# Performance work log

Measured on AMD Instinct MI355X. Metric: run time of the kernel, lower is better.

## Reference

```python
import jax, jax.numpy as jnp
import numpy as np

TEMPERATURE = 0.1

def setup_inputs() -> dict:
    key = jax.random.key(0)
    ks = jax.random.split(key, 6)
    B, K, D, H, N = 256, 32, 128, 256, 16
    z = jax.random.normal(ks[0], (B, K, D), dtype=jnp.float32)
    # edge MLP params: Linear(2D->H), GELU, Linear(H->D)
    W1 = jax.random.normal(ks[1], (2 * D, H), dtype=jnp.float32) * (1.0 / np.sqrt(2 * D))
    b1 = jnp.zeros((H,), dtype=jnp.float32)
    W2 = jax.random.normal(ks[2], (H, D), dtype=jnp.float32) * (1.0 / np.sqrt(H))
    b2 = jnp.zeros((D,), dtype=jnp.float32)
    codebook = jax.random.normal(ks[3], (N, D), dtype=jnp.float32) * 0.02
    return {"z": z, "W1": W1, "b1": b1, "W2": W2, "b2": b2, "codebook": codebook}

def reference(z, W1, b1, W2, b2, codebook):
    # z: (B,K,D). Edge MLP on concat([z_i, z_j]) == split-weight GEMMs,
    # avoiding materializing the (B,K,K,2D) concat tensor.
    D = z.shape[-1]
    h_i = jnp.einsum('bkd,dh->bkh', z, W1[:D])   # contribution of z_i
    h_j = jnp.einsum('bkd,dh->bkh', z, W1[D:])   # contribution of z_j
    h = h_i[:, :, None, :] + h_j[:, None, :, :] + b1       # (B,K,K,H)
    h = jax.nn.gelu(h, approximate=False)                    # torch nn.GELU default = exact erf
    e_ij = jnp.einsum('bijh,hd->bijd', h, W2) + b2           # (B,K,K,D)
    logits = jnp.einsum('bijd,nd->bijn', e_ij, codebook) / TEMPERATURE  # (B,K,K,N)
    alpha_ij = jax.nn.softmax(logits, axis=-1)
    m_ij = jnp.einsum('bijn,nd->bijd', alpha_ij, codebook)   # (B,K,K,D)
    return (m_ij, alpha_ij, e_ij, logits)
```

## Files before the change

### kernel.cpp

```cpp
#include <hip/hip_runtime.h>
#include <hip/hip_bf16.h>
#include <math.h>

#define BB 256
#define KK 32
#define DD 128
#define HH 256
#define NN 16
#define O0 ((size_t)0)
#define O1 ((size_t)33554432)
#define O2 ((size_t)37748736)
#define O3 ((size_t)71303168)

typedef float f32x4 __attribute__((ext_vector_type(4)));
typedef short s16x8 __attribute__((ext_vector_type(8)));

static __device__ __forceinline__ short f2bf(float x) {
  __hip_bfloat16 h = __float2bfloat16(x);
  return *reinterpret_cast<short*>(&h);
}
static __device__ __forceinline__ float bf2f(short s) {
  __hip_bfloat16 h;
  *reinterpret_cast<short*>(&h) = s;
  return __bfloat162float(h);
}
static __device__ __forceinline__ unsigned cvt_pk_bf16(float a, float b) {
  unsigned r;
  asm volatile("v_cvt_pk_bf16_f32 %0, %1, %2" : "=v"(r) : "v"(a), "v"(b));
  return r;
}

static __device__ __forceinline__ float gelu_exact(float x) {
  float ax = fabsf(x) * 0.70710678118654752f;
  float t = __builtin_amdgcn_rcpf(fmaf(0.3275911f, ax, 1.0f));
  float p = fmaf(1.061405429f, t, -1.453152027f);
  p = fmaf(p, t, 1.421413741f);
  p = fmaf(p, t, -0.284496736f);
  p = fmaf(p, t, 0.254829592f);
  p *= t;
  float e = __expf(-ax * ax);
  float er = fmaf(-p, e, 1.0f);
  er = copysignf(er, x);
  return 0.5f * x * (1.0f + er);
}

__global__ __launch_bounds__(256) void prep_kernel(
    const float* __restrict__ z, const float* __restrict__ W1,
    const float* __restrict__ W2, const float* __restrict__ cb,
    short* __restrict__ zb, short* __restrict__ W1th, short* __restrict__ W1tl,
    short* __restrict__ Wh, short* __restrict__ Wl,
    short* __restrict__ cbh, short* __restrict__ cbl, short* __restrict__ cbT) {
  const int idx = blockIdx.x * 256 + threadIdx.x;
  zb[idx] = f2bf(z[idx]);
  if (idx < 512 * 128) {
    int c = idx >> 7, k = idx & 127;
    float w = (c < 256) ? W1[(size_t)k * 256 + c]
                        : W1[(size_t)(128 + k) * 256 + (c - 256)];
    short h = f2bf(w);
    W1th[idx] = h;
    W1tl[idx] = f2bf(w - bf2f(h));
  }
  if (idx < 128 * 256) {
    int c = idx >> 8, k = idx & 255;
    float w = W2[(size_t)k * 128 + c];
    short h = f2bf(w);
    Wh[idx] = h;
    Wl[idx] = f2bf(w - bf2f(h));
  }
  if (idx < 2048) {
    float v = cb[idx];
    short h = f2bf(v);
    cbh[idx] = h;
    cbl[idx] = f2bf(v - bf2f(h));
  }
  if (idx < 128 * 32) {
    int c = idx >> 5, n = idx & 31;
    cbT[idx] = (n < 16) ? f2bf(cb[(size_t)n * 128 + c]) : (short)0;
  }
}

__global__ __launch_bounds__(256) void hproj_mfma(
    const short* __restrict__ zb, const short* __restrict__ W1th,
    const short* __restrict__ W1tl, const float* __restrict__ b1,
    float* __restrict__ H) {
  const int tid = threadIdx.x;
  const int lane = tid & 63;
  const int wv = tid >> 6;
  const int l4 = lane >> 4, l15 = lane & 15;
  const int row0 = blockIdx.x * 32;
  const int col0 = blockIdx.y * 128 + wv * 32;

  f32x4 acc[2][2];
#pragma unroll
  for (int mt = 0; mt < 2; ++mt)
#pragma unroll
    for (int nt = 0; nt < 2; ++nt)
      acc[mt][nt] = (f32x4){0.f, 0.f, 0.f, 0.f};

#pragma unroll
  for (int ks = 0; ks < 4; ++ks) {
    const int kof = ks * 32 + l4 * 8;
    s16x8 a0 = *(const s16x8*)(zb + (size_t)(row0 + l15) * 128 + kof);
    s16x8 a1 = *(const s16x8*)(zb + (size_t)(row0 + 16 + l15) * 128 + kof);
    s16x8 bh0 = *(const s16x8*)(W1th + (size_t)(col0 + l15) * 128 + kof);
    s16x8 bh1 = *(const s16x8*)(W1th + (size_t)(col0 + 16 + l15) * 128 + kof);
    s16x8 bl0 = *(const s16x8*)(W1tl + (size_t)(col0 + l15) * 128 + kof);
    s16x8 bl1 = *(const s16x8*)(W1tl + (size_t)(col0 + 16 + l15) * 128 + kof);
    acc[0][0] = __builtin_amdgcn_mfma_f32_16x16x32_bf16(a0, bh0, acc[0][0], 0, 0, 0);
    acc[0][0] = __builtin_amdgcn_mfma_f32_16x16x32_bf16(a0, bl0, acc[0][0], 0, 0, 0);
    acc[0][1] = __builtin_amdgcn_mfma_f32_16x16x32_bf16(a0, bh1, acc[0][1], 0, 0, 0);
    acc[0][1] = __builtin_amdgcn_mfma_f32_16x16x32_bf16(a0, bl1, acc[0][1], 0, 0, 0);
    acc[1][0] = __builtin_amdgcn_mfma_f32_16x16x32_bf16(a1, bh0, acc[1][0], 0, 0, 0);
    acc[1][0] = __builtin_amdgcn_mfma_f32_16x16x32_bf16(a1, bl0, acc[1][0], 0, 0, 0);
    acc[1][1] = __builtin_amdgcn_mfma_f32_16x16x32_bf16(a1, bh1, acc[1][1], 0, 0, 0);
    acc[1][1] = __builtin_amdgcn_mfma_f32_16x16x32_bf16(a1, bl1, acc[1][1], 0, 0, 0);
  }

#pragma unroll
  for (int nt = 0; nt < 2; ++nt) {
    const int col = col0 + nt * 16 + l15;
    const float bias = (col0 < 256) ? b1[col] : 0.f;
#pragma unroll
    for (int mt = 0; mt < 2; ++mt)
#pragma unroll
      for (int r = 0; r < 4; ++r)
        H[(size_t)(row0 + mt * 16 + l4 * 4 + r) * 512 + col] =
            acc[mt][nt][r] + bias;
  }
}

__global__ __launch_bounds__(256, 4) void pair_kernel(
    const float* __restrict__ Hcat, const short* __restrict__ Wh,
    const short* __restrict__ Wl, const float* __restrict__ b2,
    const short* __restrict__ cbh, const short* __restrict__ cbl,
    const short* __restrict__ cbT, float* __restrict__ out) {
  __shared__ short sAh[32 * 256];
  __shared__ union {
    short Al[32 * 256];
    struct { short Eh[32 * 128]; short El[32 * 128]; } e;
  } u;
  __shared__ short sAlp[32 * 32];

  const int tid = threadIdx.x;
  const int blk = blockIdx.x;
  const int b = blk >> 5;

  ((unsigned*)sAlp)[tid] = 0u;
  ((unsigned*)sAlp)[tid + 256] = 0u;

  {
    const int k0 = (tid & 127) * 2;
    const int pb = (tid >> 7) * 16;
    const float2 hiv = *(const float2*)(Hcat + (size_t)blk * 512 + k0);
    const float hx = hiv.x;
    const float hy = hiv.y;
    const float* hjp = Hcat + ((size_t)b * KK + pb) * 512 + 256 + k0;
    unsigned* aH = (unsigned*)sAh;
    unsigned* aL = (unsigned*)u.Al;
    const int cw = tid & 127;
#pragma unroll 4
    for (int p = 0; p < 16; ++p) {
      const int row = pb + p;
      float2 hj = *(const float2*)(hjp + (size_t)p * 512);
      float g0 = gelu_exact(hx + hj.x);
      float g1 = gelu_exact(hy + hj.y);
      unsigned h01 = cvt_pk_bf16(g0, g1);
      float h0f = __uint_as_float(h01 << 16);
      float h1f = __uint_as_float(h01 & 0xFFFF0000u);
      unsigned l01 = cvt_pk_bf16(g0 - h0f, g1 - h1f);
      const int wi = row * 128 + ((cw ^ ((row & 7) << 2)));
      aH[wi] = h01;
      aL[wi] = l01;
    }
  }
  __syncthreads();

  const int lane = tid & 63;
  const int wv = tid >> 6;
  const int nb = wv * 32;
  const int l4 = lane >> 4;
  const int l15 = lane & 15;

  f32x4 acc[2][2];
#pragma unroll
  for (int mt = 0; mt < 2; ++mt)
#pragma unroll
    for (int nt = 0; nt < 2; ++nt)
      acc[mt][nt] = (f32x4){0.f, 0.f, 0.f, 0.f};

  const int sw = (l15 & 7) << 4;
  const char* pAh = (const char*)sAh;
  const char* pAl = (const char*)u.Al;
  const size_t gB0 = (size_t)(nb + l15) * 256 + l4 * 8;

#pragma unroll
  for (int ks = 0; ks < 8; ++ks) {
    const int cbyte = ks * 64 + l4 * 16;
    const int o0 = l15 * 512 + (cbyte ^ sw);
    const int o1 = (16 + l15) * 512 + (cbyte ^ sw);
    s16x8 ah0 = *(const s16x8*)(pAh + o0);
    s16x8 ah1 = *(const s16x8*)(pAh + o1);
    s16x8 al0 = *(const s16x8*)(pAl + o0);
    s16x8 al1 = *(const s16x8*)(pAl + o1);
    const size_t g0 = gB0 + ks * 32;
    const size_t g1 = g0 + 16 * 256;
    s16x8 bh0 = *(const s16x8*)(Wh + g0);
    s16x8 bh1 = *(const s16x8*)(Wh + g1);
    s16x8 bl0 = *(const s16x8*)(Wl + g0);
    s16x8 bl1 = *(const s16x8*)(Wl + g1);

    acc[0][0] = __builtin_amdgcn_mfma_f32_16x16x32_bf16(ah0, bh0, acc[0][0], 0, 0, 0);
    acc[0][0] = __builtin_amdgcn_mfma_f32_16x16x32_bf16(al0, bh0, acc[0][0], 0, 0, 0);
    acc[0][0] = __builtin_amdgcn_mfma_f32_16x16x32_bf16(ah0, bl0, acc[0][0], 0, 0, 0);
    acc[0][1] = __builtin_amdgcn_mfma_f32_16x16x32_bf16(ah0, bh1, acc[0][1], 0, 0, 0);
    acc[0][1] = __builtin_amdgcn_mfma_f32_16x16x32_bf16(al0, bh1, acc[0][1], 0, 0, 0);
    acc[0][1] = __builtin_amdgcn_mfma_f32_16x16x32_bf16(ah0, bl1, acc[0][1], 0, 0, 0);
    acc[1][0] = __builtin_amdgcn_mfma_f32_16x16x32_bf16(ah1, bh0, acc[1][0], 0, 0, 0);
    acc[1][0] = __builtin_amdgcn_mfma_f32_16x16x32_bf16(al1, bh0, acc[1][0], 0, 0, 0);
    acc[1][0] = __builtin_amdgcn_mfma_f32_16x16x32_bf16(ah1, bl0, acc[1][0], 0, 0, 0);
    acc[1][1] = __builtin_amdgcn_mfma_f32_16x16x32_bf16(ah1, bh1, acc[1][1], 0, 0, 0);
    acc[1][1] = __builtin_amdgcn_mfma_f32_16x16x32_bf16(al1, bh1, acc[1][1], 0, 0, 0);
    acc[1][1] = __builtin_amdgcn_mfma_f32_16x16x32_bf16(ah1, bl1, acc[1][1], 0, 0, 0);
  }

  __syncthreads();

  {
    const float b2v0 = b2[nb + l15];
    const float b2v1 = b2[nb + 16 + l15];
    float* eg = out + O2 + (size_t)blk * (KK * DD);
    char* pEh = (char*)u.e.Eh;
    char* pEl = (char*)u.e.El;
#pragma unroll
    for (int mt = 0; mt < 2; ++mt) {
#pragma unroll
      for (int r = 0; r < 4; ++r) {
        const int row = mt * 16 + l4 * 4 + r;
        const int rsw = (row & 7) << 4;
        const float e0 = acc[mt][0][r] + b2v0;
        const float e1 = acc[mt][1][r] + b2v1;
        eg[row * 128 + nb + l15] = e0;
        eg[row * 128 + nb + 16 + l15] = e1;
        unsigned hp = cvt_pk_bf16(e0, e1);
        float h0f = __uint_as_float(hp << 16);
        float h1f = __uint_as_float(hp & 0xFFFF0000u);
        unsigned lp = cvt_pk_bf16(e0 - h0f, e1 - h1f);
        const int i0 = row * 256 + (((nb + l15) * 2) ^ rsw);
        const int i1 = row * 256 + (((nb + 16 + l15) * 2) ^ rsw);
        *(short*)(pEh + i0) = (short)(hp & 0xFFFFu);
        *(short*)(pEh + i1) = (short)(hp >> 16);
        *(short*)(pEl + i0) = (short)(lp & 0xFFFFu);
        *(short*)(pEl + i1) = (short)(lp >> 16);
      }
    }
  }
  __syncthreads();

  if (wv < 2) {
    const int mrow = wv * 16;
    f32x4 lacc = (f32x4){0.f, 0.f, 0.f, 0.f};
    const char* pEh = (const char*)u.e.Eh;
    const char* pEl = (const char*)u.e.El;
    const int rowa = mrow + l15;
    const int rsw = (rowa & 7) << 4;
#pragma unroll
    for (int ks = 0; ks < 4; ++ks) {
      const int cbyte = ks * 64 + l4 * 16;
      const int o = rowa * 256 + (cbyte ^ rsw);
      s16x8 eh = *(const s16x8*)(pEh + o);
      s16x8 el = *(const s16x8*)(pEl + o);
      const size_t g = (size_t)l15 * 128 + ks * 32 + l4 * 8;
      s16x8 ch = *(const s16x8*)(cbh + g);
      s16x8 cl = *(const s16x8*)(cbl + g);
      lacc = __builtin_amdgcn_mfma_f32_16x16x32_bf16(eh, ch, lacc, 0, 0, 0);
      lacc = __builtin_amdgcn_mfma_f32_16x16x32_bf16(el, ch, lacc, 0, 0, 0);
      lacc = __builtin_amdgcn_mfma_f32_16x16x32_bf16(eh, cl, lacc, 0, 0, 0);
    }
    float* lg_out = out + O3 + (size_t)blk * (KK * NN);
    float* ag_out = out + O1 + (size_t)blk * (KK * NN);
#pragma unroll
    for (int r = 0; r < 4; ++r) {
      const int row = mrow + l4 * 4 + r;
      float lg = lacc[r] * 10.0f;
      float mx = lg;
#pragma unroll
      for (int m = 1; m < 16; m <<= 1) mx = fmaxf(mx, __shfl_xor(mx, m));
      float p = __expf(lg - mx);
      float s = p;
#pragma unroll
      for (int m = 1; m < 16; m <<= 1) s += __shfl_xor(s, m);
      float a = p / s;
      lg_out[row * 16 + l15] = lg;
      ag_out[row * 16 + l15] = a;
      sAlp[row * 32 + l15] = f2bf(a);
    }
  }
  __syncthreads();

  {
    float* mg = out + O0 + (size_t)blk * (KK * DD);
#pragma unroll
    for (int rg = 0; rg < 2; ++rg) {
      s16x8 af = *(const s16x8*)(sAlp + (rg * 16 + l15) * 32 + l4 * 8);
#pragma unroll
      for (int nt = 0; nt < 2; ++nt) {
        const int c = nb + nt * 16 + l15;
        s16x8 bf = *(const s16x8*)(cbT + (size_t)c * 32 + l4 * 8);
        f32x4 mac = (f32x4){0.f, 0.f, 0.f, 0.f};
        mac = __builtin_amdgcn_mfma_f32_16x16x32_bf16(af, bf, mac, 0, 0, 0);
#pragma unroll
        for (int r = 0; r < 4; ++r)
          mg[(rg * 16 + l4 * 4 + r) * 128 + c] = mac[r];
      }
    }
  }
}

extern "C" void kernel_launch(void* const* d_in, const int* in_sizes, int n_in,
                              void* d_out, int out_size, void* d_ws, size_t ws_size,
                              hipStream_t stream) {
  const float* z  = (const float*)d_in[0];
  const float* W1 = (const float*)d_in[1];
  const float* b1 = (const float*)d_in[2];
  const float* W2 = (const float*)d_in[3];
  const float* b2 = (const float*)d_in[4];
  const float* cb = (const float*)d_in[5];
  float* out = (float*)d_out;

  float* Hcat = (float*)d_ws;
  short* zb   = (short*)(Hcat + (size_t)8192 * 512);
  short* W1th = zb + (size_t)1048576;
  short* W1tl = W1th + (size_t)65536;
  short* Wh   = W1tl + (size_t)65536;
  short* Wl   = Wh + (size_t)32768;
  short* cbh  = Wl + (size_t)32768;
  short* cbl  = cbh + (size_t)2048;
  short* cbT  = cbl + (size_t)2048;

  prep_kernel<<<4096, 256, 0, stream>>>(z, W1, W2, cb, zb, W1th, W1tl, Wh, Wl,
                                        cbh, cbl, cbT);
  hproj_mfma<<<dim3(256, 4), 256, 0, stream>>>(zb, W1th, W1tl, b1, Hcat);
  pair_kernel<<<BB * KK, 256, 0, stream>>>(Hcat, Wh, Wl, b2, cbh, cbl, cbT, out);
}
```

Baseline: 201.1 us.

## Fold W2·codebookᵀ into a precomputed matrix to compute logits directly from GELU activations

Precomputes V = W2·codebookᵀ (256x16) and b2·codebookᵀ in the prep kernel, so the pair kernel computes logits straight from the GELU tile inside the main MFMA loop. This removes the bf16 hi/lo staging of e_ij in shared memory, the second GEMM phase and two block barriers. The cost is extra MFMAs per k-step in every wave (each wave computes a redundant logit tile that only half the lanes store), larger LDS use since the union is gone, and lower occupancy from launch bounds changing 4 to 3. The per-thread serial 128-length dot products in the prep kernel add a small amount of work there.

```diff
diff --git a/kernel.cpp b/kernel.cpp
--- a/kernel.cpp
+++ b/kernel.cpp
@@ -47,9 +47,10 @@
 __global__ __launch_bounds__(256) void prep_kernel(
     const float* __restrict__ z, const float* __restrict__ W1,
     const float* __restrict__ W2, const float* __restrict__ cb,
+    const float* __restrict__ b2,
     short* __restrict__ zb, short* __restrict__ W1th, short* __restrict__ W1tl,
-    short* __restrict__ Wh, short* __restrict__ Wl,
-    short* __restrict__ cbh, short* __restrict__ cbl, short* __restrict__ cbT) {
+    short* __restrict__ Wh, short* __restrict__ Wl, short* __restrict__ cbT,
+    short* __restrict__ Vh, short* __restrict__ Vl, float* __restrict__ b2cb) {
   const int idx = blockIdx.x * 256 + threadIdx.x;
   zb[idx] = f2bf(z[idx]);
   if (idx < 512 * 128) {
@@ -67,15 +68,24 @@
     Wh[idx] = h;
     Wl[idx] = f2bf(w - bf2f(h));
   }
-  if (idx < 2048) {
-    float v = cb[idx];
-    short h = f2bf(v);
-    cbh[idx] = h;
-    cbl[idx] = f2bf(v - bf2f(h));
-  }
   if (idx < 128 * 32) {
     int c = idx >> 5, n = idx & 31;
     cbT[idx] = (n < 16) ? f2bf(cb[(size_t)n * 128 + c]) : (short)0;
+  }
+  if (idx < 16 * 256) {
+    int n = idx >> 8, k = idx & 255;
+    float s = 0.f;
+#pragma unroll 4
+    for (int c = 0; c < 128; ++c)
+      s += W2[(size_t)k * 128 + c] * cb[(size_t)n * 128 + c];
+    short h = f2bf(s);
+    Vh[idx] = h;
+    Vl[idx] = f2bf(s - bf2f(h));
+  }
+  if (idx < 16) {
+    float s = 0.f;
+    for (int c = 0; c < 128; ++c) s += b2[c] * cb[(size_t)idx * 128 + c];
+    b2cb[idx] = s;
   }
 }
 
@@ -129,16 +139,14 @@
   }
 }
 
-__global__ __launch_bounds__(256, 4) void pair_kernel(
+__global__ __launch_bounds__(256, 3) void pair_kernel(
     const float* __restrict__ Hcat, const short* __restrict__ Wh,
     const short* __restrict__ Wl, const float* __restrict__ b2,
-    const short* __restrict__ cbh, const short* __restrict__ cbl,
-    const short* __restrict__ cbT, float* __restrict__ out) {
+    const short* __restrict__ Vh, const short* __restrict__ Vl,
+    const float* __restrict__ b2cb, const short* __restrict__ cbT,
+    float* __restrict__ out) {
   __shared__ short sAh[32 * 256];
-  __shared__ union {
-    short Al[32 * 256];
-    struct { short Eh[32 * 128]; short El[32 * 128]; } e;
-  } u;
+  __shared__ short sAl[32 * 256];
   __shared__ short sAlp[32 * 32];
 
   const int tid = threadIdx.x;
@@ -156,7 +164,7 @@
     const float hy = hiv.y;
     const float* hjp = Hcat + ((size_t)b * KK + pb) * 512 + 256 + k0;
     unsigned* aH = (unsigned*)sAh;
-    unsigned* aL = (unsigned*)u.Al;
+    unsigned* aL = (unsigned*)sAl;
     const int cw = tid & 127;
 #pragma unroll 4
     for (int p = 0; p < 16; ++p) {
@@ -180,6 +188,7 @@
   const int nb = wv * 32;
   const int l4 = lane >> 4;
   const int l15 = lane & 15;
+  const int mtL = wv >> 1;
 
   f32x4 acc[2][2];
 #pragma unroll
@@ -187,11 +196,13 @@
 #pragma unroll
     for (int nt = 0; nt < 2; ++nt)
       acc[mt][nt] = (f32x4){0.f, 0.f, 0.f, 0.f};
+  f32x4 lacc = (f32x4){0.f, 0.f, 0.f, 0.f};
 
   const int sw = (l15 & 7) << 4;
   const char* pAh = (const char*)sAh;
-  const char* pAl = (const char*)u.Al;
+  const char* pAl = (const char*)sAl;
   const size_t gB0 = (size_t)(nb + l15) * 256 + l4 * 8;
+  const size_t gV0 = (size_t)l15 * 256 + l4 * 8;
 
 #pragma unroll
   for (int ks = 0; ks < 8; ++ks) {
@@ -221,67 +232,40 @@
     acc[1][1] = __builtin_amdgcn_mfma_f32_16x16x32_bf16(ah1, bh1, acc[1][1], 0, 0, 0);
     acc[1][1] = __builtin_amdgcn_mfma_f32_16x16x32_bf16(al1, bh1, acc[1][1], 0, 0, 0);
     acc[1][1] = __builtin_amdgcn_mfma_f32_16x16x32_bf16(ah1, bl1, acc[1][1], 0, 0, 0);
-  }
-
-  __syncthreads();
+
+    s16x8 vh = *(const s16x8*)(Vh + gV0 + ks * 32);
+    s16x8 vl = *(const s16x8*)(Vl + gV0 + ks * 32);
+    s16x8 aHm = mtL ? ah1 : ah0;
+    s16x8 aLm = mtL ? al1 : al0;
+    lacc = __builtin_amdgcn_mfma_f32_16x16x32_bf16(aHm, vh, lacc, 0, 0, 0);
+    lacc = __builtin_amdgcn_mfma_f32_16x16x32_bf16(aLm, vh, lacc, 0, 0, 0);
+    lacc = __builtin_amdgcn_mfma_f32_16x16x32_bf16(aHm, vl, lacc, 0, 0, 0);
+  }
 
   {
     const float b2v0 = b2[nb + l15];
     const float b2v1 = b2[nb + 16 + l15];
     float* eg = out + O2 + (size_t)blk * (KK * DD);
-    char* pEh = (char*)u.e.Eh;
-    char* pEl = (char*)u.e.El;
 #pragma unroll
     for (int mt = 0; mt < 2; ++mt) {
 #pragma unroll
       for (int r = 0; r < 4; ++r) {
         const int row = mt * 16 + l4 * 4 + r;
-        const int rsw = (row & 7) << 4;
-        const float e0 = acc[mt][0][r] + b2v0;
-        const float e1 = acc[mt][1][r] + b2v1;
-        eg[row * 128 + nb + l15] = e0;
-        eg[row * 128 + nb + 16 + l15] = e1;
-        unsigned hp = cvt_pk_bf16(e0, e1);
-        float h0f = __uint_as_float(hp << 16);
-        float h1f = __uint_as_float(hp & 0xFFFF0000u);
-        unsigned lp = cvt_pk_bf16(e0 - h0f, e1 - h1f);
-        const int i0 = row * 256 + (((nb + l15) * 2) ^ rsw);
-        const int i1 = row * 256 + (((nb + 16 + l15) * 2) ^ rsw);
-        *(short*)(pEh + i0) = (short)(hp & 0xFFFFu);
-        *(short*)(pEh + i1) = (short)(hp >> 16);
-        *(short*)(pEl + i0) = (short)(lp & 0xFFFFu);
-        *(short*)(pEl + i1) = (short)(lp >> 16);
+        eg[row * 128 + nb + l15] = acc[mt][0][r] + b2v0;
+        eg[row * 128 + nb + 16 + l15] = acc[mt][1][r] + b2v1;
       }
     }
   }
-  __syncthreads();
-
-  if (wv < 2) {
-    const int mrow = wv * 16;
-    f32x4 lacc = (f32x4){0.f, 0.f, 0.f, 0.f};
-    const char* pEh = (const char*)u.e.Eh;
-    const char* pEl = (const char*)u.e.El;
-    const int rowa = mrow + l15;
-    const int rsw = (rowa & 7) << 4;
-#pragma unroll
-    for (int ks = 0; ks < 4; ++ks) {
-      const int cbyte = ks * 64 + l4 * 16;
-      const int o = rowa * 256 + (cbyte ^ rsw);
-      s16x8 eh = *(const s16x8*)(pEh + o);
-      s16x8 el = *(const s16x8*)(pEl + o);
-      const size_t g = (size_t)l15 * 128 + ks * 32 + l4 * 8;
-      s16x8 ch = *(const s16x8*)(cbh + g);
-      s16x8 cl = *(const s16x8*)(cbl + g);
-      lacc = __builtin_amdgcn_mfma_f32_16x16x32_bf16(eh, ch, lacc, 0, 0, 0);
-      lacc = __builtin_amdgcn_mfma_f32_16x16x32_bf16(el, ch, lacc, 0, 0, 0);
-      lacc = __builtin_amdgcn_mfma_f32_16x16x32_bf16(eh, cl, lacc, 0, 0, 0);
-    }
+
+  {
+    const float b2cbv = b2cb[l15];
+    const bool own = ((l4 >> 1) == (wv & 1));
     float* lg_out = out + O3 + (size_t)blk * (KK * NN);
     float* ag_out = out + O1 + (size_t)blk * (KK * NN);
 #pragma unroll
     for (int r = 0; r < 4; ++r) {
-      const int row = mrow + l4 * 4 + r;
-      float lg = lacc[r] * 10.0f;
+      const int row = mtL * 16 + l4 * 4 + r;
+      float lg = (lacc[r] + b2cbv) * 10.0f;
       float mx = lg;
 #pragma unroll
       for (int m = 1; m < 16; m <<= 1) mx = fmaxf(mx, __shfl_xor(mx, m));
@@ -290,9 +274,11 @@
 #pragma unroll
       for (int m = 1; m < 16; m <<= 1) s += __shfl_xor(s, m);
       float a = p / s;
-      lg_out[row * 16 + l15] = lg;
-      ag_out[row * 16 + l15] = a;
-      sAlp[row * 32 + l15] = f2bf(a);
+      if (own) {
+        lg_out[row * 16 + l15] = lg;
+        ag_out[row * 16 + l15] = a;
+        sAlp[row * 32 + l15] = f2bf(a);
+      }
     }
   }
   __syncthreads();
@@ -333,12 +319,13 @@
   short* W1tl = W1th + (size_t)65536;
   short* Wh   = W1tl + (size_t)65536;
   short* Wl   = Wh + (size_t)32768;
-  short* cbh  = Wl + (size_t)32768;
-  short* cbl  = cbh + (size_t)2048;
-  short* cbT  = cbl + (size_t)2048;
-
-  prep_kernel<<<4096, 256, 0, stream>>>(z, W1, W2, cb, zb, W1th, W1tl, Wh, Wl,
-                                        cbh, cbl, cbT);
+  short* cbT  = Wl + (size_t)32768;
+  short* Vh   = cbT + (size_t)4096;
+  short* Vl   = Vh + (size_t)4096;
+  float* b2cb = (float*)(Vl + (size_t)4096);
+
+  prep_kernel<<<4096, 256, 0, stream>>>(z, W1, W2, cb, b2, zb, W1th, W1tl, Wh,
+                                        Wl, cbT, Vh, Vl, b2cb);
   hproj_mfma<<<dim3(256, 4), 256, 0, stream>>>(zb, W1th, W1tl, b1, Hcat);
-  pair_kernel<<<BB * KK, 256, 0, stream>>>(Hcat, Wh, Wl, b2, cbh, cbl, cbT, out);
-}
+  pair_kernel<<<BB * KK, 256, 0, stream>>>(Hcat, Wh, Wl, b2, Vh, Vl, b2cb, cbT, out);
+}
```

Result: slower. 243.9 us (+21.3%).
